# Kernel tuning notes

Measured on AMD Instinct MI355X. Metric: run time of the kernel, lower is better.

The kernel has to match this reference:

```python
import jax, jax.numpy as jnp
import numpy as np

IN_F = 4096
OUT_F = 4096
ROWS = 8192  # batch*seq


def setup_inputs() -> dict:
    key = jax.random.key(0)
    k1, k2, k3 = jax.random.split(key, 3)
    scale = (2.0 / IN_F) ** 0.5
    x = jax.random.normal(k1, (ROWS, IN_F), dtype=jnp.float32)
    weight_real = jax.random.normal(k2, (OUT_F, IN_F), dtype=jnp.float32) * scale
    weight_imag = jax.random.normal(k3, (OUT_F, IN_F), dtype=jnp.float32) * scale
    bias = jnp.zeros((OUT_F,), dtype=jnp.float32)
    return {"x": x, "weight_real": weight_real, "weight_imag": weight_imag, "bias": bias}


def reference(x, weight_real, weight_imag, bias):
    # complex matmul with real input x: out_c = x @ (Wr + i Wi)^T
    real = jnp.matmul(x, weight_real.T)   # [rows, out]
    imag = jnp.matmul(x, weight_imag.T)   # [rows, out]
    magnitude = jnp.sqrt(real * real + imag * imag)  # torch.abs(out_c)
    phase = jnp.arctan2(imag, real)                   # torch.angle(out_c)
    interference = jnp.cos(phase)
    return magnitude * interference + bias
```

## Files before the change

### kernel.cpp

```cpp
#include <hip/hip_runtime.h>
#include <hip/hip_bf16.h>
#include <cstdint>
#include <cstddef>


#define TILE 128
#define BK 32

typedef short bf16x8 __attribute__((ext_vector_type(8)));
typedef float f32x4 __attribute__((ext_vector_type(4)));

__device__ __forceinline__ unsigned short f2bf(float f) {
  unsigned int x = __float_as_uint(f);
  unsigned int r = x + 0x7FFFu + ((x >> 16) & 1u);
  return (unsigned short)(r >> 16);
}

__global__ void cvt_f32_to_bf16(const float* __restrict__ src,
                                unsigned short* __restrict__ dst, int n8) {
  int i = blockIdx.x * blockDim.x + threadIdx.x;
  int stride = gridDim.x * blockDim.x;
  for (; i < n8; i += stride) {
    float4 a = ((const float4*)src)[2 * i];
    float4 b = ((const float4*)src)[2 * i + 1];
    union { unsigned short u[8]; uint4 v; } o;
    o.u[0] = f2bf(a.x); o.u[1] = f2bf(a.y);
    o.u[2] = f2bf(a.z); o.u[3] = f2bf(a.w);
    o.u[4] = f2bf(b.x); o.u[5] = f2bf(b.y);
    o.u[6] = f2bf(b.z); o.u[7] = f2bf(b.w);
    ((uint4*)dst)[i] = o.v;
  }
}

template <bool DIRECT>
__global__ void gemm_bt_bf16(const unsigned short* __restrict__ Abf,
                             const unsigned short* __restrict__ Bbf,
                             const float* __restrict__ Afp,
                             const float* __restrict__ Bfp,
                             const float* __restrict__ bias,
                             float* __restrict__ C,
                             int M, int N, int K) {
  __shared__ unsigned short Als[TILE * BK];
  __shared__ unsigned short Bls[TILE * BK];

  const int tid = threadIdx.x;
  const int wave = tid >> 6;
  const int lane = tid & 63;
  const int lrow = lane & 15;
  const int quad = lane >> 4;
  const int mW = (wave >> 1) * 64;
  const int nW = (wave & 1) * 64;
  const int row0 = blockIdx.y * TILE;
  const int col0 = blockIdx.x * TILE;

  f32x4 acc[4][4];
  const f32x4 zero = {0.f, 0.f, 0.f, 0.f};
#pragma unroll
  for (int i = 0; i < 4; ++i)
#pragma unroll
    for (int j = 0; j < 4; ++j) acc[i][j] = zero;

  for (int k0 = 0; k0 < K; k0 += BK) {
    if (DIRECT) {
#pragma unroll
      for (int c = 0; c < 2; ++c) {
        int e = c * 256 + tid;
        int r = e >> 2;
        int kc = (e & 3) * 8;
        const unsigned short* ga = Abf + (size_t)(row0 + r) * K + k0 + kc;
        const unsigned short* gb = Bbf + (size_t)(col0 + r) * K + k0 + kc;
        unsigned short* la = Als + (size_t)(c * 256 + wave * 64) * 8;
        unsigned short* lb = Bls + (size_t)(c * 256 + wave * 64) * 8;
        __builtin_amdgcn_global_load_lds(
            (const __attribute__((address_space(1))) void*)ga,
            (__attribute__((address_space(3))) void*)la, 16, 0, 0);
        __builtin_amdgcn_global_load_lds(
            (const __attribute__((address_space(1))) void*)gb,
            (__attribute__((address_space(3))) void*)lb, 16, 0, 0);
      }
    } else {
#pragma unroll
      for (int c = 0; c < 2; ++c) {
        int e0 = c * 2048 + tid * 8;
        int r = e0 >> 5;
        int kc = e0 & 31;
        const float* ga = Afp + (size_t)(row0 + r) * K + k0 + kc;
        const float* gb = Bfp + (size_t)(col0 + r) * K + k0 + kc;
        float4 a0 = ((const float4*)ga)[0];
        float4 a1 = ((const float4*)ga)[1];
        float4 b0 = ((const float4*)gb)[0];
        float4 b1 = ((const float4*)gb)[1];
        union { unsigned short u[8]; uint4 v; } oa, ob;
        oa.u[0] = f2bf(a0.x); oa.u[1] = f2bf(a0.y);
        oa.u[2] = f2bf(a0.z); oa.u[3] = f2bf(a0.w);
        oa.u[4] = f2bf(a1.x); oa.u[5] = f2bf(a1.y);
        oa.u[6] = f2bf(a1.z); oa.u[7] = f2bf(a1.w);
        ob.u[0] = f2bf(b0.x); ob.u[1] = f2bf(b0.y);
        ob.u[2] = f2bf(b0.z); ob.u[3] = f2bf(b0.w);
        ob.u[4] = f2bf(b1.x); ob.u[5] = f2bf(b1.y);
        ob.u[6] = f2bf(b1.z); ob.u[7] = f2bf(b1.w);
        *(uint4*)&Als[e0] = oa.v;
        *(uint4*)&Bls[e0] = ob.v;
      }
    }
    __syncthreads();

    bf16x8 af[4], bfr[4];
#pragma unroll
    for (int t = 0; t < 4; ++t) {
      af[t] = *(const bf16x8*)&Als[(mW + t * 16 + lrow) * BK + quad * 8];
      bfr[t] = *(const bf16x8*)&Bls[(nW + t * 16 + lrow) * BK + quad * 8];
    }
#pragma unroll
    for (int mt = 0; mt < 4; ++mt)
#pragma unroll
      for (int nt = 0; nt < 4; ++nt)
        acc[mt][nt] = __builtin_amdgcn_mfma_f32_16x16x32_bf16(
            af[mt], bfr[nt], acc[mt][nt], 0, 0, 0);
    __syncthreads();
  }

#pragma unroll
  for (int nt = 0; nt < 4; ++nt) {
    int col = col0 + nW + nt * 16 + lrow;
    float bv = bias[col];
#pragma unroll
    for (int mt = 0; mt < 4; ++mt) {
      int rowb = row0 + mW + mt * 16 + quad * 4;
#pragma unroll
      for (int r = 0; r < 4; ++r) {
        C[(size_t)(rowb + r) * N + col] = acc[mt][nt][r] + bv;
      }
    }
  }
}

extern "C" void kernel_launch(void* const* d_in, const int* in_sizes, int n_in,
                              void* d_out, int out_size, void* d_ws, size_t ws_size,
                              hipStream_t stream) {
  const int M = 8192, N = 4096, K = 4096;
  const float* x = (const float*)d_in[0];
  const float* wr = (const float*)d_in[1];
  const float* bias = (const float*)d_in[3];
  float* out = (float*)d_out;

  const size_t nA = (size_t)M * K;
  const size_t nB = (size_t)N * K;
  dim3 grid(N / TILE, M / TILE);

  if (ws_size >= (nA + nB) * sizeof(unsigned short)) {
    unsigned short* xa = (unsigned short*)d_ws;
    unsigned short* wb = xa + nA;
    hipLaunchKernelGGL(cvt_f32_to_bf16, dim3(2048), dim3(256), 0, stream,
                       x, xa, (int)(nA / 8));
    hipLaunchKernelGGL(cvt_f32_to_bf16, dim3(1024), dim3(256), 0, stream,
                       wr, wb, (int)(nB / 8));
    hipLaunchKernelGGL((gemm_bt_bf16<true>), grid, dim3(256), 0, stream,
                       xa, wb, (const float*)nullptr, (const float*)nullptr,
                       bias, out, M, N, K);
  } else {
    hipLaunchKernelGGL((gemm_bt_bf16<false>), grid, dim3(256), 0, stream,
                       (const unsigned short*)nullptr, (const unsigned short*)nullptr,
                       x, wr, bias, out, M, N, K);
  }
}
```

Baseline: 590.5 us.

## Double K tile depth to 64 and merge the two bf16 conversion launches

Raises the per-iteration K slice from 32 to 64. Each block now loads twice as much data into LDS per barrier pair and issues two MFMA sub-steps per iteration, halving the loop trip count and synchronisation overhead. The two fp32-to-bf16 conversion kernels are merged into a single launch that covers both the activations and the weights. The larger LDS footprint (32 KB) may reduce blocks per CU, and the wider row stride may change LDS bank conflict behaviour.

```diff
diff --git a/kernel.cpp b/kernel.cpp
--- a/kernel.cpp
+++ b/kernel.cpp
@@ -5,7 +5,7 @@
 
 
 #define TILE 128
-#define BK 32
+#define BK 64
 
 typedef short bf16x8 __attribute__((ext_vector_type(8)));
 typedef float f32x4 __attribute__((ext_vector_type(4)));
@@ -16,19 +16,26 @@
   return (unsigned short)(r >> 16);
 }
 
-__global__ void cvt_f32_to_bf16(const float* __restrict__ src,
-                                unsigned short* __restrict__ dst, int n8) {
+__global__ void cvt_both_f32_to_bf16(const float* __restrict__ x,
+                                     const float* __restrict__ wr,
+                                     unsigned short* __restrict__ xa,
+                                     unsigned short* __restrict__ wb,
+                                     int nA8, int nB8) {
   int i = blockIdx.x * blockDim.x + threadIdx.x;
   int stride = gridDim.x * blockDim.x;
-  for (; i < n8; i += stride) {
-    float4 a = ((const float4*)src)[2 * i];
-    float4 b = ((const float4*)src)[2 * i + 1];
+  int total = nA8 + nB8;
+  for (; i < total; i += stride) {
+    const float* src; unsigned short* dst; int j;
+    if (i < nA8) { src = x;  dst = xa; j = i; }
+    else         { src = wr; dst = wb; j = i - nA8; }
+    float4 a = ((const float4*)src)[2 * j];
+    float4 b = ((const float4*)src)[2 * j + 1];
     union { unsigned short u[8]; uint4 v; } o;
     o.u[0] = f2bf(a.x); o.u[1] = f2bf(a.y);
     o.u[2] = f2bf(a.z); o.u[3] = f2bf(a.w);
     o.u[4] = f2bf(b.x); o.u[5] = f2bf(b.y);
     o.u[6] = f2bf(b.z); o.u[7] = f2bf(b.w);
-    ((uint4*)dst)[i] = o.v;
+    ((uint4*)dst)[j] = o.v;
   }
 }
 
@@ -63,10 +70,10 @@
   for (int k0 = 0; k0 < K; k0 += BK) {
     if (DIRECT) {
 #pragma unroll
-      for (int c = 0; c < 2; ++c) {
+      for (int c = 0; c < 4; ++c) {
         int e = c * 256 + tid;
-        int r = e >> 2;
-        int kc = (e & 3) * 8;
+        int r = e >> 3;
+        int kc = (e & 7) * 8;
         const unsigned short* ga = Abf + (size_t)(row0 + r) * K + k0 + kc;
         const unsigned short* gb = Bbf + (size_t)(col0 + r) * K + k0 + kc;
         unsigned short* la = Als + (size_t)(c * 256 + wave * 64) * 8;
@@ -80,10 +87,10 @@
       }
     } else {
 #pragma unroll
-      for (int c = 0; c < 2; ++c) {
-        int e0 = c * 2048 + tid * 8;
-        int r = e0 >> 5;
-        int kc = e0 & 31;
+      for (int c = 0; c < 4; ++c) {
+        int e0 = (c * 256 + tid) * 8;
+        int r = e0 >> 6;
+        int kc = e0 & 63;
         const float* ga = Afp + (size_t)(row0 + r) * K + k0 + kc;
         const float* gb = Bfp + (size_t)(col0 + r) * K + k0 + kc;
         float4 a0 = ((const float4*)ga)[0];
@@ -105,18 +112,21 @@
     }
     __syncthreads();
 
-    bf16x8 af[4], bfr[4];
 #pragma unroll
-    for (int t = 0; t < 4; ++t) {
-      af[t] = *(const bf16x8*)&Als[(mW + t * 16 + lrow) * BK + quad * 8];
-      bfr[t] = *(const bf16x8*)&Bls[(nW + t * 16 + lrow) * BK + quad * 8];
+    for (int h = 0; h < 2; ++h) {
+      bf16x8 af[4], bfr[4];
+#pragma unroll
+      for (int t = 0; t < 4; ++t) {
+        af[t]  = *(const bf16x8*)&Als[(mW + t * 16 + lrow) * BK + h * 32 + quad * 8];
+        bfr[t] = *(const bf16x8*)&Bls[(nW + t * 16 + lrow) * BK + h * 32 + quad * 8];
+      }
+#pragma unroll
+      for (int mt = 0; mt < 4; ++mt)
+#pragma unroll
+        for (int nt = 0; nt < 4; ++nt)
+          acc[mt][nt] = __builtin_amdgcn_mfma_f32_16x16x32_bf16(
+              af[mt], bfr[nt], acc[mt][nt], 0, 0, 0);
     }
-#pragma unroll
-    for (int mt = 0; mt < 4; ++mt)
-#pragma unroll
-      for (int nt = 0; nt < 4; ++nt)
-        acc[mt][nt] = __builtin_amdgcn_mfma_f32_16x16x32_bf16(
-            af[mt], bfr[nt], acc[mt][nt], 0, 0, 0);
     __syncthreads();
   }
 
@@ -151,10 +161,8 @@
   if (ws_size >= (nA + nB) * sizeof(unsigned short)) {
     unsigned short* xa = (unsigned short*)d_ws;
     unsigned short* wb = xa + nA;
-    hipLaunchKernelGGL(cvt_f32_to_bf16, dim3(2048), dim3(256), 0, stream,
-                       x, xa, (int)(nA / 8));
-    hipLaunchKernelGGL(cvt_f32_to_bf16, dim3(1024), dim3(256), 0, stream,
-                       wr, wb, (int)(nB / 8));
+    hipLaunchKernelGGL(cvt_both_f32_to_bf16, dim3(4096), dim3(256), 0, stream,
+                       x, wr, xa, wb, (int)(nA / 8), (int)(nB / 8));
     hipLaunchKernelGGL((gemm_bt_bf16<true>), grid, dim3(256), 0, stream,
                        xa, wb, (const float*)nullptr, (const float*)nullptr,
                        bias, out, M, N, K);
```

Measured after the change: 577.1 us. -2.3%, faster.
